# Performance work log

Measured on AMD Instinct MI355X. Metric: run time of the kernel, lower is better.

## Reference

```python
import jax, jax.numpy as jnp
import numpy as np

KERNEL = 3

def setup_inputs() -> dict:
    key = jax.random.key(0)
    k1, k2 = jax.random.split(key)
    x = jax.random.normal(k1, (32, 64, 64, 64), dtype=jnp.float32)
    weights = jax.random.normal(k2, (128, 64, KERNEL * KERNEL), dtype=jnp.float32)
    return {"x": x, "weights": weights}

def reference(x, weights):
    # x: (B, C, H, W); weights: (OC, C, k*k) with torch-unfold ordering
    # (channel slowest, kernel row-major) -> reshape to OIHW conv kernel.
    B, C, H, W = x.shape
    OC = weights.shape[0]
    wk = weights.reshape(OC, C, KERNEL, KERNEL)
    # stride-1, dilation-1, VALID conv == the unfold + per-(oc,c) matmul sum
    y = jax.lax.conv_general_dilated(
        x, wk, window_strides=(1, 1), padding="VALID",
        dimension_numbers=("NCHW", "OIHW", "NCHW"))
    Ho, Wo = y.shape[2], y.shape[3]
    # Faithful replication of the original's layout bug: results are laid out
    # as [oc*B + b] then reinterpreted via view(B, OC, Ho, Wo).
    y = jnp.transpose(y, (1, 0, 2, 3)).reshape(B, OC, Ho, Wo)
    return y
```

## Files before the change

kernel.cpp:

```cpp
#include <hip/hip_runtime.h>


typedef __attribute__((ext_vector_type(8))) short short8;
typedef __attribute__((ext_vector_type(16))) float f32x16;
typedef __attribute__((ext_vector_type(4))) unsigned int uint4v;

__device__ __forceinline__ unsigned short f2bf(float f) {
    unsigned u = __builtin_bit_cast(unsigned, f);
    u = (u + 0x7FFFu + ((u >> 16) & 1u)) >> 16;
    return (unsigned short)u;
}

__device__ __forceinline__ void glds16(const void* g, void* s) {
    __builtin_amdgcn_global_load_lds(
        (const __attribute__((address_space(1))) unsigned int*)g,
        (__attribute__((address_space(3))) unsigned int*)s, 16, 0, 0);
}

__global__ __launch_bounds__(256)
void transpose_x(const float* __restrict__ x, char* __restrict__ xT) {
    __shared__ float tile[64][65];
    const int tid = threadIdx.x;
    const int h = blockIdx.x, b = blockIdx.y;

    #pragma unroll
    for (int i = 0; i < 4; ++i) {
        const int idx = i * 256 + tid;
        const int c = idx >> 4, j = idx & 15;
        const float4 v = *(const float4*)(x + (size_t)(((b * 64 + c) * 64 + h) * 64 + j * 4));
        tile[c][j * 4 + 0] = v.x; tile[c][j * 4 + 1] = v.y;
        tile[c][j * 4 + 2] = v.z; tile[c][j * 4 + 3] = v.w;
    }
    __syncthreads();

    #pragma unroll
    for (int i = 0; i < 2; ++i) {
        const int idx = i * 256 + tid;
        const int col = idx >> 3, q = idx & 7;
        unsigned int wds[4];
        #pragma unroll
        for (int jj = 0; jj < 4; ++jj) {
            const unsigned short lo = f2bf(tile[q * 8 + 2 * jj + 0][col]);
            const unsigned short hi = f2bf(tile[q * 8 + 2 * jj + 1][col]);
            wds[jj] = (unsigned)lo | ((unsigned)hi << 16);
        }
        uint4v v; v[0] = wds[0]; v[1] = wds[1]; v[2] = wds[2]; v[3] = wds[3];
        *(uint4v*)(xT + (size_t)(((b * 64 + h) * 64 + col) * 128) + ((q ^ (col & 7)) * 16)) = v;
    }
}

__global__ __launch_bounds__(256)
void pack_w(const float* __restrict__ w, char* __restrict__ wT) {
    const int id = blockIdx.x * 256 + threadIdx.x;
    const int t = id >> 10;
    const int rem = id & 1023;
    const int oc = rem >> 3, q = rem & 7;
    unsigned int wds[4];
    #pragma unroll
    for (int jj = 0; jj < 4; ++jj) {
        const unsigned short lo = f2bf(w[(size_t)oc * 576 + (q * 8 + 2 * jj + 0) * 9 + t]);
        const unsigned short hi = f2bf(w[(size_t)oc * 576 + (q * 8 + 2 * jj + 1) * 9 + t]);
        wds[jj] = (unsigned)lo | ((unsigned)hi << 16);
    }
    uint4v v; v[0] = wds[0]; v[1] = wds[1]; v[2] = wds[2]; v[3] = wds[3];
    *(uint4v*)(wT + (size_t)(t * 16384 + oc * 128) + ((q ^ (oc & 7)) * 16)) = v;
}

#define ROWSTRIDE 8448

__global__ __launch_bounds__(256, 2)
void quanv_mfma32(const char* __restrict__ xT, const char* __restrict__ wT,
                  float* __restrict__ out) {
    __shared__ __align__(16) char sx[6 * ROWSTRIDE];

    const int tid  = threadIdx.x;
    const int lane = tid & 63;
    const int wid  = tid >> 6;
    const int hot  = blockIdx.x;
    const int b    = blockIdx.y;
    const int ho0  = hot * 4;

    for (int k = wid; k < 48; k += 4) {
        const int r = k >> 3, sub = k & 7;
        int gr = ho0 + r; if (gr > 63) gr = 63;
        glds16(xT + (size_t)((b * 64 + gr) * 8192 + sub * 1024 + lane * 16),
               sx + r * ROWSTRIDE + sub * 1024);
    }
    __syncthreads();

    const int l31 = lane & 31;
    const int hi  = lane >> 5;
    const int ho  = ho0 + wid;

    int voff[4];
    #pragma unroll
    for (int kc = 0; kc < 4; ++kc)
        voff[kc] = l31 * 128 + (((kc * 2 + hi) ^ (l31 & 7)) * 16);

    f32x16 acc[4][2];
    #pragma unroll
    for (int mt = 0; mt < 4; ++mt)
        #pragma unroll
        for (int nt = 0; nt < 2; ++nt)
            #pragma unroll
            for (int e = 0; e < 16; ++e) acc[mt][nt][e] = 0.f;

    #pragma unroll
    for (int tap = 0; tap < 9; ++tap) {
        const int kh = tap / 3, kw = tap % 3;
        const char* wtap = wT + (size_t)tap * 16384;

        short8 a[4][4];
        #pragma unroll
        for (int kc = 0; kc < 4; ++kc)
            #pragma unroll
            for (int mt = 0; mt < 4; ++mt)
                a[kc][mt] = *(const short8*)(wtap + mt * 4096 + voff[kc]);

        const int colswz = (kw + l31) & 7;
        const int bbase  = (wid + kh) * ROWSTRIDE + (kw + l31) * 128;
        #pragma unroll
        for (int kc = 0; kc < 4; ++kc) {
            short8 bf[2];
            #pragma unroll
            for (int nt = 0; nt < 2; ++nt)
                bf[nt] = *(const short8*)(sx + bbase + nt * 4096 +
                                          (((kc * 2 + hi) ^ colswz) * 16));
            #pragma unroll
            for (int mt = 0; mt < 4; ++mt)
                #pragma unroll
                for (int nt = 0; nt < 2; ++nt)
                    acc[mt][nt] = __builtin_amdgcn_mfma_f32_32x32x16_bf16(
                        a[kc][mt], bf[nt], acc[mt][nt], 0, 0, 0);
        }
    }

    if (ho < 62) {
        #pragma unroll
        for (int mt = 0; mt < 4; ++mt) {
            #pragma unroll
            for (int r = 0; r < 16; ++r) {
                const int oc = mt * 32 + (r & 3) + 8 * (r >> 2) + 4 * hi;
                float* op = out + ((size_t)(oc * 32 + b) * 62 + ho) * 62;
                op[l31] = acc[mt][0][r];
                if (l31 < 30) op[32 + l31] = acc[mt][1][r];
            }
        }
    }
}

#define CCH   8
#define OC_PT 8
#define ROWS  18
__global__ __launch_bounds__(256, 4)
void quanv_f32(const float* __restrict__ x, const float* __restrict__ w,
               float* __restrict__ out) {
    __shared__ float sx_raw[CCH * ROWS * 64 + 4];
    #define SX(cl, row, col) sx_raw[((cl) * ROWS + (row)) * 64 + (col)]
    const int tid = threadIdx.x;
    const int tx = tid & 15, ty = tid >> 4;
    const int hot = blockIdx.x, ocg = blockIdx.y, b = blockIdx.z;
    const int row0 = hot * 16, ho = row0 + ty, wo0 = tx * 4;
    const float* xb = x + (size_t)b * (64 * 64 * 64);
    const float* wb = w + (size_t)(ocg * OC_PT) * 576;
    float acc[OC_PT][4];
    #pragma unroll
    for (int o = 0; o < OC_PT; ++o)
        #pragma unroll
        for (int q = 0; q < 4; ++q) acc[o][q] = 0.f;
    for (int cc = 0; cc < 64; cc += CCH) {
        __syncthreads();
        #pragma unroll
        for (int j = 0; j < 9; ++j) {
            const int idx = j * 256 + tid;
            const int col4 = idx & 15, rowc = idx >> 4;
            const int row = rowc % ROWS, cl = rowc / ROWS;
            int gr = row0 + row; if (gr > 63) gr = 63;
            *(float4*)(&sx_raw[idx * 4]) =
                *(const float4*)(xb + ((size_t)(cc + cl) * 64 + gr) * 64 + col4 * 4);
        }
        __syncthreads();
        for (int cl = 0; cl < CCH; ++cl) {
            float xv[3][6];
            #pragma unroll
            for (int kh = 0; kh < 3; ++kh)
                #pragma unroll
                for (int j = 0; j < 6; ++j) xv[kh][j] = SX(cl, ty + kh, wo0 + j);
            const float* wc = wb + (size_t)(cc + cl) * 9;
            #pragma unroll
            for (int o = 0; o < OC_PT; ++o) {
                float wv[9];
                #pragma unroll
                for (int t = 0; t < 9; ++t) wv[t] = wc[(size_t)o * 576 + t];
                #pragma unroll
                for (int kh = 0; kh < 3; ++kh)
                    #pragma unroll
                    for (int kw = 0; kw < 3; ++kw) {
                        const float wvv = wv[kh * 3 + kw];
                        #pragma unroll
                        for (int q = 0; q < 4; ++q)
                            acc[o][q] = fmaf(xv[kh][kw + q], wvv, acc[o][q]);
                    }
            }
        }
    }
    if (ho < 62) {
        #pragma unroll
        for (int o = 0; o < OC_PT; ++o) {
            const int oc = ocg * OC_PT + o;
            float* op = out + ((size_t)(oc * 32 + b) * 62 + ho) * 62 + wo0;
            #pragma unroll
            for (int q = 0; q < 4; ++q)
                if (wo0 + q < 62) op[q] = acc[o][q];
        }
    }
    #undef SX
}

extern "C" void kernel_launch(void* const* d_in, const int* in_sizes, int n_in,
                              void* d_out, int out_size, void* d_ws, size_t ws_size,
                              hipStream_t stream) {
    const float* x = (const float*)d_in[0];
    const float* w = (const float*)d_in[1];
    float* out = (float*)d_out;

    const size_t XT_BYTES = 16777216;
    const size_t WT_BYTES = 147456;

    if (ws_size >= XT_BYTES + WT_BYTES) {
        char* xT = (char*)d_ws;
        char* wT = (char*)d_ws + XT_BYTES;
        transpose_x<<<dim3(64, 32), 256, 0, stream>>>(x, xT);
        pack_w<<<36, 256, 0, stream>>>(w, wT);
        quanv_mfma32<<<dim3(16, 32), 256, 0, stream>>>(xT, wT, out);
    } else {
        quanv_f32<<<dim3(4, 16, 32), 256, 0, stream>>>(x, w, out);
    }
}
```

Before: 122.5 us.

## Split MFMA warps over row pairs and OC halves with prefetched weight taps

Each wave now handles two output rows and half of the output channels, instead of one row and all channels. This halves the per-wave weight fragment registers and lets each A fragment be reused across two rows. The tap loop is no longer unrolled, and the next tap's weights are software-prefetched from global memory into registers while the current tap's MFMAs run. The intent is to cut global weight traffic per wave and hide its latency. The cost is doubled LDS B-fragment reads per MFMA pair and extra loop overhead from the rolled loop.

```diff
diff --git a/kernel.cpp b/kernel.cpp
--- a/kernel.cpp
+++ b/kernel.cpp
@@ -90,60 +90,88 @@
 
     const int l31 = lane & 31;
     const int hi  = lane >> 5;
-    const int ho  = ho0 + wid;
+    const int rp  = wid >> 1;
+    const int oh  = wid & 1;
 
     int voff[4];
     #pragma unroll
     for (int kc = 0; kc < 4; ++kc)
         voff[kc] = l31 * 128 + (((kc * 2 + hi) ^ (l31 & 7)) * 16);
 
-    f32x16 acc[4][2];
-    #pragma unroll
-    for (int mt = 0; mt < 4; ++mt)
-        #pragma unroll
-        for (int nt = 0; nt < 2; ++nt)
-            #pragma unroll
-            for (int e = 0; e < 16; ++e) acc[mt][nt][e] = 0.f;
-
-    #pragma unroll
+    f32x16 acc[2][2][2];
+    #pragma unroll
+    for (int r = 0; r < 2; ++r)
+        #pragma unroll
+        for (int mtl = 0; mtl < 2; ++mtl)
+            #pragma unroll
+            for (int nt = 0; nt < 2; ++nt)
+                #pragma unroll
+                for (int e = 0; e < 16; ++e) acc[r][mtl][nt][e] = 0.f;
+
+    const char* wt0 = wT + (size_t)(oh * 2) * 4096;
+    short8 acur[4][2];
+    #pragma unroll
+    for (int kc = 0; kc < 4; ++kc)
+        #pragma unroll
+        for (int mtl = 0; mtl < 2; ++mtl)
+            acur[kc][mtl] = *(const short8*)(wt0 + mtl * 4096 + voff[kc]);
+
+    int kh = 0, kw = 0;
+    const char* wt = wt0;
+    #pragma unroll 1
     for (int tap = 0; tap < 9; ++tap) {
-        const int kh = tap / 3, kw = tap % 3;
-        const char* wtap = wT + (size_t)tap * 16384;
-
-        short8 a[4][4];
+        short8 anxt[4][2];
+        const char* wn = wt + 16384;
+        if (tap < 8) {
+            #pragma unroll
+            for (int kc = 0; kc < 4; ++kc)
+                #pragma unroll
+                for (int mtl = 0; mtl < 2; ++mtl)
+                    anxt[kc][mtl] = *(const short8*)(wn + mtl * 4096 + voff[kc]);
+        }
+
+        const int colswz = (kw + l31) & 7;
+        const int cbase  = (kw + l31) * 128;
+        #pragma unroll
+        for (int kc = 0; kc < 4; ++kc) {
+            const int chs = (((kc * 2 + hi) ^ colswz) * 16);
+            #pragma unroll
+            for (int r = 0; r < 2; ++r) {
+                const char* bp = sx + (2 * rp + r + kh) * ROWSTRIDE + cbase + chs;
+                short8 bf0 = *(const short8*)(bp);
+                short8 bf1 = *(const short8*)(bp + 4096);
+                #pragma unroll
+                for (int mtl = 0; mtl < 2; ++mtl) {
+                    acc[r][mtl][0] = __builtin_amdgcn_mfma_f32_32x32x16_bf16(
+                        acur[kc][mtl], bf0, acc[r][mtl][0], 0, 0, 0);
+                    acc[r][mtl][1] = __builtin_amdgcn_mfma_f32_32x32x16_bf16(
+                        acur[kc][mtl], bf1, acc[r][mtl][1], 0, 0, 0);
+                }
+            }
+        }
+
         #pragma unroll
         for (int kc = 0; kc < 4; ++kc)
             #pragma unroll
-            for (int mt = 0; mt < 4; ++mt)
-                a[kc][mt] = *(const short8*)(wtap + mt * 4096 + voff[kc]);
-
-        const int colswz = (kw + l31) & 7;
-        const int bbase  = (wid + kh) * ROWSTRIDE + (kw + l31) * 128;
-        #pragma unroll
-        for (int kc = 0; kc < 4; ++kc) {
-            short8 bf[2];
-            #pragma unroll
-            for (int nt = 0; nt < 2; ++nt)
-                bf[nt] = *(const short8*)(sx + bbase + nt * 4096 +
-                                          (((kc * 2 + hi) ^ colswz) * 16));
-            #pragma unroll
-            for (int mt = 0; mt < 4; ++mt)
-                #pragma unroll
-                for (int nt = 0; nt < 2; ++nt)
-                    acc[mt][nt] = __builtin_amdgcn_mfma_f32_32x32x16_bf16(
-                        a[kc][mt], bf[nt], acc[mt][nt], 0, 0, 0);
-        }
-    }
-
-    if (ho < 62) {
-        #pragma unroll
-        for (int mt = 0; mt < 4; ++mt) {
-            #pragma unroll
-            for (int r = 0; r < 16; ++r) {
-                const int oc = mt * 32 + (r & 3) + 8 * (r >> 2) + 4 * hi;
-                float* op = out + ((size_t)(oc * 32 + b) * 62 + ho) * 62;
-                op[l31] = acc[mt][0][r];
-                if (l31 < 30) op[32 + l31] = acc[mt][1][r];
+            for (int mtl = 0; mtl < 2; ++mtl)
+                acur[kc][mtl] = anxt[kc][mtl];
+        wt = wn;
+        if (++kw == 3) { kw = 0; ++kh; }
+    }
+
+    #pragma unroll
+    for (int r = 0; r < 2; ++r) {
+        const int ho = ho0 + 2 * rp + r;
+        if (ho < 62) {
+            #pragma unroll
+            for (int mtl = 0; mtl < 2; ++mtl) {
+                #pragma unroll
+                for (int g = 0; g < 16; ++g) {
+                    const int oc = (oh * 2 + mtl) * 32 + (g & 3) + 8 * (g >> 2) + 4 * hi;
+                    float* op = out + ((size_t)(oc * 32 + b) * 62 + ho) * 62;
+                    op[l31] = acc[r][mtl][0][g];
+                    if (l31 < 30) op[32 + l31] = acc[r][mtl][1][g];
+                }
             }
         }
     }
```

Result: faster. 117.7 us (-3.9%).
